# Kernel optimization log

Hardware: AMD Instinct MI355X
Metric: run time of the kernel (lower is better)

The kernel has to match this reference:

```python
import jax, jax.numpy as jnp
import numpy as np

N = 100000   # nodes
R = 8        # relations
E = 800000   # edges per relation
D = 128      # in_feat == out_feat
B = 4        # num bases
L = 2        # ngnn layers


def setup_inputs() -> dict:
    key = jax.random.key(0)
    ks = jax.random.split(key, 8)
    x = jax.random.normal(ks[0], (N, D), dtype=jnp.float32)
    edge_src = jax.random.randint(ks[1], (R, E), 0, N, dtype=jnp.int64)
    edge_dst = jax.random.randint(ks[2], (R, E), 0, N, dtype=jnp.int64)
    scale = 1.0 / np.sqrt(D)
    w_comp = jax.random.normal(ks[3], (R, B), dtype=jnp.float32) * 0.3
    bases = jax.random.normal(ks[4], (B, D, D), dtype=jnp.float32) * scale
    loop_weight = jax.random.normal(ks[5], (D, D), dtype=jnp.float32) * scale
    h_bias = jnp.zeros((D,), dtype=jnp.float32)
    ngnn_w = jax.random.normal(ks[6], (L, D, D), dtype=jnp.float32) * scale
    return {"x": x, "edge_src": edge_src, "edge_dst": edge_dst,
            "w_comp": w_comp, "bases": bases, "loop_weight": loop_weight,
            "h_bias": h_bias, "ngnn_w": ngnn_w}


def reference(x, edge_src, edge_dst, w_comp, bases, loop_weight, h_bias, ngnn_w):
    # basis-decomposed per-relation weights: [R, D, D]
    weight = jnp.einsum('rb,bio->rio', w_comp, bases)
    h = jnp.zeros((N, D), dtype=x.dtype)
    # per-relation GraphConv, norm='right' (mean over in-degree, clamp min 1),
    # in_feat == out_feat so DGL aggregates first then applies weight;
    # HeteroGraphConv sums relation outputs for the shared dst type.
    for r in range(R):
        src, dst = edge_src[r], edge_dst[r]
        msg = jax.ops.segment_sum(x[src], dst, num_segments=N)           # [N, D]
        deg = jax.ops.segment_sum(jnp.ones((E,), x.dtype), dst, num_segments=N)
        agg = msg / jnp.maximum(deg, 1.0)[:, None]
        h = h + agg @ weight[r]
    # self loop + bias + activation
    h = jax.nn.relu(h + x @ loop_weight + h_bias)
    # NGNN MLP (dropout is identity in eval)
    for l in range(ngnn_w.shape[0]):
        h = jax.nn.relu(h @ ngnn_w[l])
    return h
```

## Files before the change

kernel.cpp:

```cpp
#include <hip/hip_runtime.h>
#include <hip/hip_bf16.h>

#define N_NODES 100000
#define R_REL   8
#define E_EDGES 800000
#define D_FEAT  128
#define B_BASES 4
#define RN      (R_REL * N_NODES)
#define RE      (R_REL * E_EDGES)

#define NBKT    784
#define BKT_CAP 9216
#define P1_TPB  256
#define P1_EPT  32
#define P1_CHUNK (P1_TPB * P1_EPT)
#define P1_NWG  ((RE + P1_CHUNK - 1) / P1_CHUNK)

#define SUB_PER_BKT 4
#define SGRID   (NBKT * SUB_PER_BKT)
#define SUBCAP  2816

typedef __attribute__((ext_vector_type(8))) short short8;
typedef __attribute__((ext_vector_type(4))) float floatx4;

__global__ __launch_bounds__(1024) void init_cursor_kernel(int* __restrict__ gcursor) {
    int t = threadIdx.x;
    if (t < NBKT) gcursor[t] = t * BKT_CAP;
}

__global__ __launch_bounds__(256) void xcvt_kernel(
    const float* __restrict__ x, uint* __restrict__ xb) {
    int i = blockIdx.x * 256 + threadIdx.x;
    if (i >= N_NODES * 64) return;
    float2 v = *(const float2*)(x + 2 * (size_t)i);
    __hip_bfloat162 h = __float22bfloat162_rn(v);
    xb[i] = *(uint*)&h;
}

__global__ __launch_bounds__(256) void wcvt_kernel(
    const float* __restrict__ bases, const float* __restrict__ loopw,
    unsigned short* __restrict__ wT) {
    int idx = blockIdx.x * 256 + threadIdx.x;
    if (idx >= 128 * 640) return;
    int n = idx / 640, k = idx % 640;
    float v = (k < 512) ? bases[(size_t)k * 128 + n] : loopw[(size_t)(k - 512) * 128 + n];
    __hip_bfloat16 h = __float2bfloat16(v);
    wT[idx] = *(unsigned short*)&h;
}

__global__ __launch_bounds__(256) void wcvt2_kernel(
    const float* __restrict__ ngnn_w, unsigned short* __restrict__ wT2) {
    int idx = blockIdx.x * 256 + threadIdx.x;
    if (idx >= 2 * 128 * 128) return;
    int l = idx >> 14, rem = idx & 16383;
    int n = rem >> 7, k = rem & 127;
    float v = ngnn_w[(size_t)l * 16384 + (size_t)k * 128 + n];
    __hip_bfloat16 h = __float2bfloat16(v);
    wT2[idx] = *(unsigned short*)&h;
}

__global__ __launch_bounds__(256) void p1_kernel(
    const int* __restrict__ src, const int* __restrict__ dst,
    int* __restrict__ gcursor, int* __restrict__ ebuf2) {
    __shared__ int hist[NBKT];
    __shared__ int cnt2[NBKT];
    __shared__ int basebkt[NBKT];
    __shared__ int lofs[NBKT];
    __shared__ int aux[256];
    __shared__ int recs[P1_CHUNK];
    __shared__ unsigned short bb[P1_CHUNK];
    int t = threadIdx.x;
    for (int i = t; i < NBKT; i += 256) { hist[i] = 0; cnt2[i] = 0; }
    __syncthreads();

    int e0 = blockIdx.x * P1_CHUNK;
    int rec[P1_EPT];
    int bkt[P1_EPT];
#pragma unroll
    for (int i = 0; i < P1_EPT; ++i) {
        int e = e0 + i * P1_TPB + t;
        if (e < RE) {
            int d = dst[e];
            int s = src[e];
            int r = e / E_EDGES;
            bkt[i] = d >> 7;
            rec[i] = s | ((d & 127) << 17) | (r << 24);
            atomicAdd(&hist[bkt[i]], 1);
        } else bkt[i] = -1;
    }
    __syncthreads();

    int k0 = t * 4;
    int c0 = (k0 + 0 < NBKT) ? hist[k0 + 0] : 0;
    int c1 = (k0 + 1 < NBKT) ? hist[k0 + 1] : 0;
    int c2 = (k0 + 2 < NBKT) ? hist[k0 + 2] : 0;
    int c3 = (k0 + 3 < NBKT) ? hist[k0 + 3] : 0;
    int s1 = c0 + c1, s2 = s1 + c2, s3 = s2 + c3;
    aux[t] = s3;
    __syncthreads();
    int vv = s3;
    for (int off = 1; off < 256; off <<= 1) {
        int yv = (t >= off) ? aux[t - off] : 0;
        __syncthreads();
        vv += yv;
        aux[t] = vv;
        __syncthreads();
    }
    int total = aux[255];
    int texcl = vv - s3;
    if (k0 + 0 < NBKT) lofs[k0 + 0] = texcl;
    if (k0 + 1 < NBKT) lofs[k0 + 1] = texcl + c0;
    if (k0 + 2 < NBKT) lofs[k0 + 2] = texcl + s1;
    if (k0 + 3 < NBKT) lofs[k0 + 3] = texcl + s2;
    __syncthreads();
    for (int i = t; i < NBKT; i += 256) {
        int hv = hist[i];
        basebkt[i] = (hv > 0) ? atomicAdd(&gcursor[i], hv) : 0;
    }
    __syncthreads();

#pragma unroll
    for (int i = 0; i < P1_EPT; ++i) {
        if (bkt[i] >= 0) {
            int p = lofs[bkt[i]] + atomicAdd(&cnt2[bkt[i]], 1);
            recs[p] = rec[i];
            bb[p] = (unsigned short)bkt[i];
        }
    }
    __syncthreads();

    for (int i = t; i < total; i += 256) {
        int b = bb[i];
        int p2 = basebkt[b] + (i - lofs[b]);
        if (p2 < (b + 1) * BKT_CAP) ebuf2[p2] = recs[i];
    }
}

template <bool XB>
__global__ __launch_bounds__(512, 8) void agg3_kernel(
    const float* __restrict__ x,
    const uint*  __restrict__ xb,
    const int*   __restrict__ gcursor,
    const int*   __restrict__ ebuf2,
    const float* __restrict__ w_comp,
    __hip_bfloat162* __restrict__ y) {
    __shared__ int raw[SUBCAP];
    __shared__ int sorted[SUBCAP];
    __shared__ int cursors[256];
    __shared__ int segbeg[256];
    __shared__ int nraw;
    const int t = threadIdx.x;
    const int bucket = blockIdx.x % NBKT;
    const int sub    = blockIdx.x / NBKT;

    int cnt = gcursor[bucket] - bucket * BKT_CAP;
    if (cnt > BKT_CAP) cnt = BKT_CAP;
    const int* brec = ebuf2 + (size_t)bucket * BKT_CAP;
    if (t < 256) cursors[t] = 0;
    if (t == 0) nraw = 0;
    __syncthreads();

    const int lane = t & 63;
    const unsigned long long lmask = (1ull << lane) - 1ull;

    for (int i0 = 0; i0 < cnt; i0 += 512) {
        int i = i0 + t;
        int rec = (i < cnt) ? brec[i] : 0;
        bool match = (i < cnt) && ((((rec >> 17) & 127) >> 5) == sub);
        unsigned long long mask = __ballot(match);
        int base = 0;
        if (lane == 0) base = atomicAdd(&nraw, (int)__popcll(mask));
        base = __shfl(base, 0);
        if (match) {
            int p = base + (int)__popcll(mask & lmask);
            if (p < SUBCAP) {
                raw[p] = rec;
                int key = ((rec >> 17) & 31) * 8 + ((rec >> 24) & 7);
                atomicAdd(&cursors[key], 1);
            }
        }
    }
    __syncthreads();
    int n = nraw; if (n > SUBCAP) n = SUBCAP;

    int deg = (t < 256) ? cursors[t] : 0;
    int* aux = sorted;
    aux[t] = deg;
    __syncthreads();
    int vv = deg;
    for (int off = 1; off < 256; off <<= 1) {
        int yv = (t >= off && t < 256) ? aux[t - off] : 0;
        __syncthreads();
        vv += yv;
        aux[t] = vv;
        __syncthreads();
    }
    if (t < 256) {
        cursors[t] = vv - deg;
        segbeg[t]  = vv - deg;
    }
    __syncthreads();

    for (int i = t; i < n; i += 512) {
        int rec = raw[i];
        int key = ((rec >> 17) & 31) * 8 + ((rec >> 24) & 7);
        int pos = atomicAdd(&cursors[key], 1);
        sorted[pos] = rec & 0x1FFFF;
    }
    __syncthreads();

    const int wid = t >> 6;
    const float* xp  = x + 2 * lane;
    const uint*  xbp = xb + lane;
    for (int nn = 0; nn < 4; ++nn) {
        int nl = wid * 4 + nn;
        int node = bucket * 128 + sub * 32 + nl;
        int key0 = nl * 8;
        float2 acc[B_BASES];
#pragma unroll
        for (int b = 0; b < B_BASES; ++b) acc[b] = make_float2(0.f, 0.f);
#pragma unroll
        for (int r = 0; r < R_REL; ++r) {
            int b0 = segbeg[key0 + r];
            int e0 = cursors[key0 + r];
            int d = e0 - b0;
            float inv = 1.0f / (float)(d > 1 ? d : 1);
            float ax = 0.f, ay = 0.f;
            int i = b0;
            for (; i + 3 < e0; i += 4) {
                int s0 = sorted[i], s1 = sorted[i + 1], s2 = sorted[i + 2], s3 = sorted[i + 3];
                if (XB) {
                    uint u0 = xbp[(size_t)s0 * 64];
                    uint u1 = xbp[(size_t)s1 * 64];
                    uint u2 = xbp[(size_t)s2 * 64];
                    uint u3 = xbp[(size_t)s3 * 64];
                    ax += (__uint_as_float(u0 << 16) + __uint_as_float(u1 << 16))
                        + (__uint_as_float(u2 << 16) + __uint_as_float(u3 << 16));
                    ay += (__uint_as_float(u0 & 0xFFFF0000u) + __uint_as_float(u1 & 0xFFFF0000u))
                        + (__uint_as_float(u2 & 0xFFFF0000u) + __uint_as_float(u3 & 0xFFFF0000u));
                } else {
                    float2 a = *(const float2*)(xp + (size_t)s0 * D_FEAT);
                    float2 b = *(const float2*)(xp + (size_t)s1 * D_FEAT);
                    float2 cc = *(const float2*)(xp + (size_t)s2 * D_FEAT);
                    float2 d2 = *(const float2*)(xp + (size_t)s3 * D_FEAT);
                    ax += (a.x + b.x) + (cc.x + d2.x);
                    ay += (a.y + b.y) + (cc.y + d2.y);
                }
            }
            for (; i < e0; ++i) {
                int s = sorted[i];
                if (XB) {
                    uint u = xbp[(size_t)s * 64];
                    ax += __uint_as_float(u << 16);
                    ay += __uint_as_float(u & 0xFFFF0000u);
                } else {
                    float2 a = *(const float2*)(xp + (size_t)s * D_FEAT);
                    ax += a.x; ay += a.y;
                }
            }
#pragma unroll
            for (int b = 0; b < B_BASES; ++b) {
                float coef = w_comp[r * B_BASES + b] * inv;
                acc[b].x = fmaf(coef, ax, acc[b].x);
                acc[b].y = fmaf(coef, ay, acc[b].y);
            }
        }
        if (node < N_NODES) {
#pragma unroll
            for (int b = 0; b < B_BASES; ++b)
                y[(size_t)node * 256 + b * 64 + lane] = __float22bfloat162_rn(acc[b]);
        }
    }
}

#define TPAD 136
__global__ __launch_bounds__(256) void fused_mlp(
    const short* __restrict__ y,
    const float* __restrict__ x,
    const unsigned short* __restrict__ wT,
    const float* __restrict__ bias,
    const unsigned short* __restrict__ wT2,
    float* __restrict__ out) {
    __shared__ short tile[4][16][TPAD];
    const int wave = threadIdx.x >> 6;
    const int lane = threadIdx.x & 63;
    const int quad = lane >> 4;
    const int l16  = lane & 15;
    const int row0 = blockIdx.x * 64 + wave * 16;
    int arow = row0 + l16;
    if (arow >= N_NODES) arow = N_NODES - 1;
    short (*tl)[TPAD] = tile[wave];

    floatx4 acc[8];
#pragma unroll
    for (int nt = 0; nt < 8; ++nt) acc[nt] = (floatx4){0.f, 0.f, 0.f, 0.f};

    const short* yrow = y + (size_t)arow * 512;
    const float* xrow = x + (size_t)arow * 128;
    const int koff = quad * 8;

    for (int ks = 0; ks < 16; ++ks) {
        int k0 = ks * 32 + koff;
        short8 a = *(const short8*)(yrow + k0);
#pragma unroll
        for (int nt = 0; nt < 8; ++nt) {
            int n = nt * 16 + l16;
            short8 b = *(const short8*)((const short*)wT + (size_t)n * 640 + k0);
            acc[nt] = __builtin_amdgcn_mfma_f32_16x16x32_bf16(a, b, acc[nt], 0, 0, 0);
        }
    }
#pragma unroll
    for (int ks = 0; ks < 4; ++ks) {
        int k0 = ks * 32 + koff;
        float4 fa = *(const float4*)(xrow + k0);
        float4 fb = *(const float4*)(xrow + k0 + 4);
        union { short8 s; uint u[4]; } ua;
        __hip_bfloat162 h0 = __float22bfloat162_rn(make_float2(fa.x, fa.y));
        __hip_bfloat162 h1 = __float22bfloat162_rn(make_float2(fa.z, fa.w));
        __hip_bfloat162 h2 = __float22bfloat162_rn(make_float2(fb.x, fb.y));
        __hip_bfloat162 h3 = __float22bfloat162_rn(make_float2(fb.z, fb.w));
        ua.u[0] = *(uint*)&h0; ua.u[1] = *(uint*)&h1;
        ua.u[2] = *(uint*)&h2; ua.u[3] = *(uint*)&h3;
#pragma unroll
        for (int nt = 0; nt < 8; ++nt) {
            int n = nt * 16 + l16;
            short8 b = *(const short8*)((const short*)wT + (size_t)n * 640 + 512 + k0);
            acc[nt] = __builtin_amdgcn_mfma_f32_16x16x32_bf16(ua.s, b, acc[nt], 0, 0, 0);
        }
    }

#pragma unroll
    for (int nt = 0; nt < 8; ++nt) {
        float bs = bias[nt * 16 + l16];
#pragma unroll
        for (int i = 0; i < 4; ++i) {
            float v = fmaxf(acc[nt][i] + bs, 0.f);
            __hip_bfloat16 h = __float2bfloat16(v);
            tl[quad * 4 + i][nt * 16 + l16] = *(short*)&h;
        }
    }
    __syncthreads();

#pragma unroll
    for (int l = 0; l < 2; ++l) {
        const unsigned short* wl = wT2 + l * 16384;
        short8 af[4];
#pragma unroll
        for (int ks = 0; ks < 4; ++ks)
            af[ks] = *(const short8*)&tl[l16][ks * 32 + koff];
        floatx4 acc2[8];
#pragma unroll
        for (int nt = 0; nt < 8; ++nt) acc2[nt] = (floatx4){0.f, 0.f, 0.f, 0.f};
#pragma unroll
        for (int ks = 0; ks < 4; ++ks) {
            int k0 = ks * 32 + koff;
#pragma unroll
            for (int nt = 0; nt < 8; ++nt) {
                int n = nt * 16 + l16;
                short8 b = *(const short8*)((const short*)wl + (size_t)n * 128 + k0);
                acc2[nt] = __builtin_amdgcn_mfma_f32_16x16x32_bf16(af[ks], b, acc2[nt], 0, 0, 0);
            }
        }
        if (l == 0) {
            __syncthreads();
#pragma unroll
            for (int nt = 0; nt < 8; ++nt)
#pragma unroll
                for (int i = 0; i < 4; ++i) {
                    float v = fmaxf(acc2[nt][i], 0.f);
                    __hip_bfloat16 h = __float2bfloat16(v);
                    tl[quad * 4 + i][nt * 16 + l16] = *(short*)&h;
                }
            __syncthreads();
        } else {
#pragma unroll
            for (int nt = 0; nt < 8; ++nt) {
                int n = nt * 16 + l16;
#pragma unroll
                for (int i = 0; i < 4; ++i) {
                    int m = row0 + quad * 4 + i;
                    if (m < N_NODES)
                        out[(size_t)m * D_FEAT + n] = fmaxf(acc2[nt][i], 0.f);
                }
            }
        }
    }
}

extern "C" void kernel_launch(void* const* d_in, const int* in_sizes, int n_in,
                              void* d_out, int out_size, void* d_ws, size_t ws_size,
                              hipStream_t stream) {
    const float* x           = (const float*)d_in[0];
    const int*   edge_src    = (const int*)d_in[1];
    const int*   edge_dst    = (const int*)d_in[2];
    const float* w_comp      = (const float*)d_in[3];
    const float* bases       = (const float*)d_in[4];
    const float* loop_weight = (const float*)d_in[5];
    const float* h_bias      = (const float*)d_in[6];
    const float* ngnn_w      = (const float*)d_in[7];
    float* out = (float*)d_out;

    char* ws = (char*)d_ws;
    size_t off = 0;
    __hip_bfloat162* y = (__hip_bfloat162*)(ws + off);
    off += (size_t)N_NODES * 512 * 2;
    int* ebuf2 = (int*)(ws + off);
    off += (size_t)NBKT * BKT_CAP * 4;
    int* gcursor = (int*)(ws + off);
    off += 4096;
    unsigned short* wT = (unsigned short*)(ws + off);
    off += (size_t)128 * 640 * 2;
    unsigned short* wT2 = (unsigned short*)(ws + off);
    off += (size_t)2 * 128 * 128 * 2;
    uint* xb = (uint*)(ws + off);
    size_t xb_bytes = (size_t)N_NODES * 64 * 4;
    const bool use_bf16_x = (ws_size >= off + xb_bytes);

    const int GEMM_GRID = (N_NODES + 63) / 64;

    wcvt_kernel<<<(128 * 640 + 255) / 256, 256, 0, stream>>>(bases, loop_weight, wT);
    wcvt2_kernel<<<(2 * 128 * 128 + 255) / 256, 256, 0, stream>>>(ngnn_w, wT2);
    if (use_bf16_x)
        xcvt_kernel<<<(N_NODES * 64 + 255) / 256, 256, 0, stream>>>(x, xb);

    init_cursor_kernel<<<1, 1024, 0, stream>>>(gcursor);
    p1_kernel<<<P1_NWG, P1_TPB, 0, stream>>>(edge_src, edge_dst, gcursor, ebuf2);

    if (use_bf16_x)
        agg3_kernel<true><<<SGRID, 512, 0, stream>>>(x, xb, gcursor, ebuf2, w_comp, y);
    else
        agg3_kernel<false><<<SGRID, 512, 0, stream>>>(x, nullptr, gcursor, ebuf2, w_comp, y);

    fused_mlp<<<GEMM_GRID, 256, 0, stream>>>(
        (const short*)y, x, wT, h_bias, wT2, out);
}
```

Before: 675.4 us.

## Merge prep kernels and double rows per wave in fused MLP

Four small preprocessing launches (x to bf16, weight transposes, cursor init) become a single prep kernel, cutting launch overhead. The fused MLP now handles 32 rows per wave instead of 16, so each weight B-fragment load feeds two MFMAs. When the bf16 copy of x is available, the MLP reads it directly rather than converting fp32 x in-kernel. This doubles accumulator register use and the LDS tile size, which may lower occupancy.

New measurement: 597.3 us. -11.6%, faster.

```diff
diff --git a/kernel.cpp b/kernel.cpp
--- a/kernel.cpp
+++ b/kernel.cpp
@@ -20,43 +20,48 @@
 #define SGRID   (NBKT * SUB_PER_BKT)
 #define SUBCAP  2816
 
+#define NXW  (N_NODES * 64)
+#define NW1  (128 * 640)
+#define NW2  (2 * 128 * 128)
+
 typedef __attribute__((ext_vector_type(8))) short short8;
 typedef __attribute__((ext_vector_type(4))) float floatx4;
 
-__global__ __launch_bounds__(1024) void init_cursor_kernel(int* __restrict__ gcursor) {
-    int t = threadIdx.x;
-    if (t < NBKT) gcursor[t] = t * BKT_CAP;
-}
-
-__global__ __launch_bounds__(256) void xcvt_kernel(
-    const float* __restrict__ x, uint* __restrict__ xb) {
-    int i = blockIdx.x * 256 + threadIdx.x;
-    if (i >= N_NODES * 64) return;
-    float2 v = *(const float2*)(x + 2 * (size_t)i);
-    __hip_bfloat162 h = __float22bfloat162_rn(v);
-    xb[i] = *(uint*)&h;
-}
-
-__global__ __launch_bounds__(256) void wcvt_kernel(
+__global__ __launch_bounds__(256) void prep_kernel(
+    const float* __restrict__ x, uint* __restrict__ xb,
     const float* __restrict__ bases, const float* __restrict__ loopw,
-    unsigned short* __restrict__ wT) {
+    unsigned short* __restrict__ wT,
+    const float* __restrict__ ngnn_w, unsigned short* __restrict__ wT2,
+    int* __restrict__ gcursor, int do_x) {
     int idx = blockIdx.x * 256 + threadIdx.x;
-    if (idx >= 128 * 640) return;
-    int n = idx / 640, k = idx % 640;
-    float v = (k < 512) ? bases[(size_t)k * 128 + n] : loopw[(size_t)(k - 512) * 128 + n];
-    __hip_bfloat16 h = __float2bfloat16(v);
-    wT[idx] = *(unsigned short*)&h;
-}
-
-__global__ __launch_bounds__(256) void wcvt2_kernel(
-    const float* __restrict__ ngnn_w, unsigned short* __restrict__ wT2) {
-    int idx = blockIdx.x * 256 + threadIdx.x;
-    if (idx >= 2 * 128 * 128) return;
-    int l = idx >> 14, rem = idx & 16383;
-    int n = rem >> 7, k = rem & 127;
-    float v = ngnn_w[(size_t)l * 16384 + (size_t)k * 128 + n];
-    __hip_bfloat16 h = __float2bfloat16(v);
-    wT2[idx] = *(unsigned short*)&h;
+    if (do_x) {
+        if (idx < NXW) {
+            float2 v = *(const float2*)(x + 2 * (size_t)idx);
+            __hip_bfloat162 h = __float22bfloat162_rn(v);
+            xb[idx] = *(uint*)&h;
+            return;
+        }
+        idx -= NXW;
+    }
+    if (idx < NW1) {
+        int n = idx / 640, k = idx % 640;
+        float v = (k < 512) ? bases[(size_t)k * 128 + n]
+                            : loopw[(size_t)(k - 512) * 128 + n];
+        __hip_bfloat16 h = __float2bfloat16(v);
+        wT[idx] = *(unsigned short*)&h;
+        return;
+    }
+    idx -= NW1;
+    if (idx < NW2) {
+        int l = idx >> 14, rem = idx & 16383;
+        int n = rem >> 7, k = rem & 127;
+        float v = ngnn_w[(size_t)l * 16384 + (size_t)k * 128 + n];
+        __hip_bfloat16 h = __float2bfloat16(v);
+        wT2[idx] = *(unsigned short*)&h;
+        return;
+    }
+    idx -= NW2;
+    if (idx < NBKT) gcursor[idx] = idx * BKT_CAP;
 }
 
 __global__ __launch_bounds__(256) void p1_kernel(
@@ -274,58 +279,97 @@
 }
 
 #define TPAD 136
+template <bool XB>
 __global__ __launch_bounds__(256) void fused_mlp(
     const short* __restrict__ y,
     const float* __restrict__ x,
+    const uint*  __restrict__ xb,
     const unsigned short* __restrict__ wT,
     const float* __restrict__ bias,
     const unsigned short* __restrict__ wT2,
     float* __restrict__ out) {
-    __shared__ short tile[4][16][TPAD];
+    __shared__ short tile[4][32][TPAD];
     const int wave = threadIdx.x >> 6;
     const int lane = threadIdx.x & 63;
     const int quad = lane >> 4;
     const int l16  = lane & 15;
-    const int row0 = blockIdx.x * 64 + wave * 16;
-    int arow = row0 + l16;
-    if (arow >= N_NODES) arow = N_NODES - 1;
+    const int rbase = blockIdx.x * 128 + wave * 32;
+    int r0 = rbase + l16;      if (r0 >= N_NODES) r0 = N_NODES - 1;
+    int r1 = rbase + 16 + l16; if (r1 >= N_NODES) r1 = N_NODES - 1;
     short (*tl)[TPAD] = tile[wave];
-
-    floatx4 acc[8];
-#pragma unroll
-    for (int nt = 0; nt < 8; ++nt) acc[nt] = (floatx4){0.f, 0.f, 0.f, 0.f};
-
-    const short* yrow = y + (size_t)arow * 512;
-    const float* xrow = x + (size_t)arow * 128;
     const int koff = quad * 8;
 
+    floatx4 acc0[8], acc1[8];
+#pragma unroll
+    for (int nt = 0; nt < 8; ++nt) {
+        acc0[nt] = (floatx4){0.f, 0.f, 0.f, 0.f};
+        acc1[nt] = (floatx4){0.f, 0.f, 0.f, 0.f};
+    }
+
+    const short* y0 = y + (size_t)r0 * 512;
+    const short* y1 = y + (size_t)r1 * 512;
     for (int ks = 0; ks < 16; ++ks) {
         int k0 = ks * 32 + koff;
-        short8 a = *(const short8*)(yrow + k0);
+        short8 a0 = *(const short8*)(y0 + k0);
+        short8 a1 = *(const short8*)(y1 + k0);
 #pragma unroll
         for (int nt = 0; nt < 8; ++nt) {
             int n = nt * 16 + l16;
             short8 b = *(const short8*)((const short*)wT + (size_t)n * 640 + k0);
-            acc[nt] = __builtin_amdgcn_mfma_f32_16x16x32_bf16(a, b, acc[nt], 0, 0, 0);
-        }
-    }
-#pragma unroll
-    for (int ks = 0; ks < 4; ++ks) {
-        int k0 = ks * 32 + koff;
-        float4 fa = *(const float4*)(xrow + k0);
-        float4 fb = *(const float4*)(xrow + k0 + 4);
-        union { short8 s; uint u[4]; } ua;
-        __hip_bfloat162 h0 = __float22bfloat162_rn(make_float2(fa.x, fa.y));
-        __hip_bfloat162 h1 = __float22bfloat162_rn(make_float2(fa.z, fa.w));
-        __hip_bfloat162 h2 = __float22bfloat162_rn(make_float2(fb.x, fb.y));
-        __hip_bfloat162 h3 = __float22bfloat162_rn(make_float2(fb.z, fb.w));
-        ua.u[0] = *(uint*)&h0; ua.u[1] = *(uint*)&h1;
-        ua.u[2] = *(uint*)&h2; ua.u[3] = *(uint*)&h3;
-#pragma unroll
-        for (int nt = 0; nt < 8; ++nt) {
-            int n = nt * 16 + l16;
-            short8 b = *(const short8*)((const short*)wT + (size_t)n * 640 + 512 + k0);
-            acc[nt] = __builtin_amdgcn_mfma_f32_16x16x32_bf16(ua.s, b, acc[nt], 0, 0, 0);
+            acc0[nt] = __builtin_amdgcn_mfma_f32_16x16x32_bf16(a0, b, acc0[nt], 0, 0, 0);
+            acc1[nt] = __builtin_amdgcn_mfma_f32_16x16x32_bf16(a1, b, acc1[nt], 0, 0, 0);
+        }
+    }
+    if (XB) {
+        const short* xb0 = (const short*)xb + (size_t)r0 * 128;
+        const short* xb1 = (const short*)xb + (size_t)r1 * 128;
+#pragma unroll
+        for (int ks = 0; ks < 4; ++ks) {
+            int kl = ks * 32 + koff;
+            short8 a0 = *(const short8*)(xb0 + kl);
+            short8 a1 = *(const short8*)(xb1 + kl);
+#pragma unroll
+            for (int nt = 0; nt < 8; ++nt) {
+                int n = nt * 16 + l16;
+                short8 b = *(const short8*)((const short*)wT + (size_t)n * 640 + 512 + kl);
+                acc0[nt] = __builtin_amdgcn_mfma_f32_16x16x32_bf16(a0, b, acc0[nt], 0, 0, 0);
+                acc1[nt] = __builtin_amdgcn_mfma_f32_16x16x32_bf16(a1, b, acc1[nt], 0, 0, 0);
+            }
+        }
+    } else {
+        const float* x0 = x + (size_t)r0 * 128;
+        const float* x1 = x + (size_t)r1 * 128;
+#pragma unroll
+        for (int ks = 0; ks < 4; ++ks) {
+            int kl = ks * 32 + koff;
+            union { short8 s; uint u[4]; } ua0, ua1;
+            {
+                float4 fa = *(const float4*)(x0 + kl);
+                float4 fb = *(const float4*)(x0 + kl + 4);
+                __hip_bfloat162 h0 = __float22bfloat162_rn(make_float2(fa.x, fa.y));
+                __hip_bfloat162 h1 = __float22bfloat162_rn(make_float2(fa.z, fa.w));
+                __hip_bfloat162 h2 = __float22bfloat162_rn(make_float2(fb.x, fb.y));
+                __hip_bfloat162 h3 = __float22bfloat162_rn(make_float2(fb.z, fb.w));
+                ua0.u[0] = *(uint*)&h0; ua0.u[1] = *(uint*)&h1;
+                ua0.u[2] = *(uint*)&h2; ua0.u[3] = *(uint*)&h3;
+            }
+            {
+                float4 fa = *(const float4*)(x1 + kl);
+                float4 fb = *(const float4*)(x1 + kl + 4);
+                __hip_bfloat162 h0 = __float22bfloat162_rn(make_float2(fa.x, fa.y));
+                __hip_bfloat162 h1 = __float22bfloat162_rn(make_float2(fa.z, fa.w));
+                __hip_bfloat162 h2 = __float22bfloat162_rn(make_float2(fb.x, fb.y));
+                __hip_bfloat162 h3 = __float22bfloat162_rn(make_float2(fb.z, fb.w));
+                ua1.u[0] = *(uint*)&h0; ua1.u[1] = *(uint*)&h1;
+                ua1.u[2] = *(uint*)&h2; ua1.u[3] = *(uint*)&h3;
+            }
+#pragma unroll
+            for (int nt = 0; nt < 8; ++nt) {
+                int n = nt * 16 + l16;
+                short8 b = *(const short8*)((const short*)wT + (size_t)n * 640 + 512 + kl);
+                acc0[nt] = __builtin_amdgcn_mfma_f32_16x16x32_bf16(ua0.s, b, acc0[nt], 0, 0, 0);
+                acc1[nt] = __builtin_amdgcn_mfma_f32_16x16x32_bf16(ua1.s, b, acc1[nt], 0, 0, 0);
+            }
         }
     }
 
@@ -334,9 +378,13 @@
         float bs = bias[nt * 16 + l16];
 #pragma unroll
         for (int i = 0; i < 4; ++i) {
-            float v = fmaxf(acc[nt][i] + bs, 0.f);
-            __hip_bfloat16 h = __float2bfloat16(v);
-            tl[quad * 4 + i][nt * 16 + l16] = *(short*)&h;
+            int row = quad * 4 + i;
+            float v0 = fmaxf(acc0[nt][i] + bs, 0.f);
+            float v1 = fmaxf(acc1[nt][i] + bs, 0.f);
+            __hip_bfloat16 h0 = __float2bfloat16(v0);
+            __hip_bfloat16 h1 = __float2bfloat16(v1);
+            tl[row][nt * 16 + l16]      = *(short*)&h0;
+            tl[16 + row][nt * 16 + l16] = *(short*)&h1;
         }
     }
     __syncthreads();
@@ -344,13 +392,18 @@
 #pragma unroll
     for (int l = 0; l < 2; ++l) {
         const unsigned short* wl = wT2 + l * 16384;
-        short8 af[4];
-#pragma unroll
-        for (int ks = 0; ks < 4; ++ks)
-            af[ks] = *(const short8*)&tl[l16][ks * 32 + koff];
-        floatx4 acc2[8];
-#pragma unroll
-        for (int nt = 0; nt < 8; ++nt) acc2[nt] = (floatx4){0.f, 0.f, 0.f, 0.f};
+        short8 af0[4], af1[4];
+#pragma unroll
+        for (int ks = 0; ks < 4; ++ks) {
+            af0[ks] = *(const short8*)&tl[l16][ks * 32 + koff];
+            af1[ks] = *(const short8*)&tl[16 + l16][ks * 32 + koff];
+        }
+        floatx4 ac0[8], ac1[8];
+#pragma unroll
+        for (int nt = 0; nt < 8; ++nt) {
+            ac0[nt] = (floatx4){0.f, 0.f, 0.f, 0.f};
+            ac1[nt] = (floatx4){0.f, 0.f, 0.f, 0.f};
+        }
 #pragma unroll
         for (int ks = 0; ks < 4; ++ks) {
             int k0 = ks * 32 + koff;
@@ -358,7 +411,8 @@
             for (int nt = 0; nt < 8; ++nt) {
                 int n = nt * 16 + l16;
                 short8 b = *(const short8*)((const short*)wl + (size_t)n * 128 + k0);
-                acc2[nt] = __builtin_amdgcn_mfma_f32_16x16x32_bf16(af[ks], b, acc2[nt], 0, 0, 0);
+                ac0[nt] = __builtin_amdgcn_mfma_f32_16x16x32_bf16(af0[ks], b, ac0[nt], 0, 0, 0);
+                ac1[nt] = __builtin_amdgcn_mfma_f32_16x16x32_bf16(af1[ks], b, ac1[nt], 0, 0, 0);
             }
         }
         if (l == 0) {
@@ -367,9 +421,13 @@
             for (int nt = 0; nt < 8; ++nt)
 #pragma unroll
                 for (int i = 0; i < 4; ++i) {
-                    float v = fmaxf(acc2[nt][i], 0.f);
-                    __hip_bfloat16 h = __float2bfloat16(v);
-                    tl[quad * 4 + i][nt * 16 + l16] = *(short*)&h;
+                    int row = quad * 4 + i;
+                    float v0 = fmaxf(ac0[nt][i], 0.f);
+                    float v1 = fmaxf(ac1[nt][i], 0.f);
+                    __hip_bfloat16 h0 = __float2bfloat16(v0);
+                    __hip_bfloat16 h1 = __float2bfloat16(v1);
+                    tl[row][nt * 16 + l16]      = *(short*)&h0;
+                    tl[16 + row][nt * 16 + l16] = *(short*)&h1;
                 }
             __syncthreads();
         } else {
@@ -378,9 +436,12 @@
                 int n = nt * 16 + l16;
 #pragma unroll
                 for (int i = 0; i < 4; ++i) {
-                    int m = row0 + quad * 4 + i;
-                    if (m < N_NODES)
-                        out[(size_t)m * D_FEAT + n] = fmaxf(acc2[nt][i], 0.f);
+                    int m0 = rbase + quad * 4 + i;
+                    int m1 = rbase + 16 + quad * 4 + i;
+                    if (m0 < N_NODES)
+                        out[(size_t)m0 * D_FEAT + n] = fmaxf(ac0[nt][i], 0.f);
+                    if (m1 < N_NODES)
+                        out[(size_t)m1 * D_FEAT + n] = fmaxf(ac1[nt][i], 0.f);
                 }
             }
         }
@@ -416,14 +477,10 @@
     size_t xb_bytes = (size_t)N_NODES * 64 * 4;
     const bool use_bf16_x = (ws_size >= off + xb_bytes);
 
-    const int GEMM_GRID = (N_NODES + 63) / 64;
-
-    wcvt_kernel<<<(128 * 640 + 255) / 256, 256, 0, stream>>>(bases, loop_weight, wT);
-    wcvt2_kernel<<<(2 * 128 * 128 + 255) / 256, 256, 0, stream>>>(ngnn_w, wT2);
-    if (use_bf16_x)
-        xcvt_kernel<<<(N_NODES * 64 + 255) / 256, 256, 0, stream>>>(x, xb);
-
-    init_cursor_kernel<<<1, 1024, 0, stream>>>(gcursor);
+    int prep_items = (use_bf16_x ? NXW : 0) + NW1 + NW2 + NBKT;
+    prep_kernel<<<(prep_items + 255) / 256, 256, 0, stream>>>(
+        x, xb, bases, loop_weight, wT, ngnn_w, wT2, gcursor, use_bf16_x ? 1 : 0);
+
     p1_kernel<<<P1_NWG, P1_TPB, 0, stream>>>(edge_src, edge_dst, gcursor, ebuf2);
 
     if (use_bf16_x)
@@ -431,6 +488,11 @@
     else
         agg3_kernel<false><<<SGRID, 512, 0, stream>>>(x, nullptr, gcursor, ebuf2, w_comp, y);
 
-    fused_mlp<<<GEMM_GRID, 256, 0, stream>>>(
-        (const short*)y, x, wT, h_bias, wT2, out);
+    const int MLP_GRID = (N_NODES + 127) / 128;
+    if (use_bf16_x)
+        fused_mlp<true><<<MLP_GRID, 256, 0, stream>>>(
+            (const short*)y, x, xb, wT, h_bias, wT2, out);
+    else
+        fused_mlp<false><<<MLP_GRID, 256, 0, stream>>>(
+            (const short*)y, x, nullptr, wT, h_bias, wT2, out);
 }
```
